# Performance work log

Measured on AMD Instinct MI355X. Metric: run time of the kernel, lower is better.

## Reference

```python
import jax, jax.numpy as jnp
import numpy as np

B, SQ, SK, H, A = 4, 512, 512, 256, 128

def setup_inputs() -> dict:
    key = jax.random.key(0)
    ks = jax.random.split(key, 8)
    s = 1.0 / np.sqrt(H)
    sa = 1.0 / np.sqrt(A)
    return {
        "Q": jax.random.normal(ks[0], (B, SQ, H), dtype=jnp.float32),
        "K": jax.random.normal(ks[1], (B, SK, H), dtype=jnp.float32),
        "V": jax.random.normal(ks[2], (B, SK, H), dtype=jnp.float32),
        "W_q": jax.random.uniform(ks[3], (H, A), jnp.float32, -s, s),
        "W_k": jax.random.uniform(ks[4], (H, A), jnp.float32, -s, s),
        "v": jax.random.uniform(ks[5], (A,), jnp.float32, -sa, sa),
        "W_o": jax.random.uniform(ks[6], (H, H), jnp.float32, -s, s),
        "b_o": jax.random.uniform(ks[7], (H,), jnp.float32, -s, s),
    }

def reference(Q, K, V, W_q, W_k, v, W_o, b_o):
    # Q: (B, Sq, H), K/V: (B, Sk, H)
    Qt = Q @ W_q                      # (B, Sq, A)
    Kt = K @ W_k                      # (B, Sk, A)
    additive = jnp.tanh(Qt[:, :, None, :] + Kt[:, None, :, :])  # (B, Sq, Sk, A)
    scores = jnp.einsum('bqka,a->bqk', additive, v)             # (B, Sq, Sk)
    weights = jax.nn.softmax(scores, axis=-1)                   # (B, Sq, Sk)
    out = jnp.einsum('bqk,bkh->bqh', weights, V)                 # (B, Sq, H)
    out = out @ W_o + b_o
    return (out, weights)
```

## Files before the change

kernel.cpp:

```cpp
#include <hip/hip_runtime.h>
#include <math.h>

#define BB 4
#define SQL 512
#define SKL 512
#define HH 256
#define AA 128

#define PRESCALE 2.8853900817779268f
#define LOG2E    1.4426950408889634f

__device__ inline void fma4(float4& a, float s, const float4& b) {
    a.x = fmaf(s, b.x, a.x); a.y = fmaf(s, b.y, a.y);
    a.z = fmaf(s, b.z, a.z); a.w = fmaf(s, b.w, a.w);
}

template <int CTRL>
__device__ __forceinline__ float dpp_add(float x) {
    int m = __builtin_amdgcn_update_dpp(__float_as_int(x), __float_as_int(x),
                                        CTRL, 0xF, 0xF, false);
    return x + __int_as_float(m);
}
__device__ __forceinline__ float red8(float x) {
    x = dpp_add<0xB1>(x);
    x = dpp_add<0x4E>(x);
    x = dpp_add<0x141>(x);
    return x;
}

__global__ __launch_bounds__(256) void prep_kernel(
    const float* __restrict__ Q, const float* __restrict__ K,
    const float* __restrict__ V,
    const float* __restrict__ Wq, const float* __restrict__ Wk,
    const float* __restrict__ Wo,
    float* __restrict__ Qt, float* __restrict__ Kt, float* __restrict__ VW)
{
    __shared__ float rows[16 * HH];
    __shared__ float wl[64 * 128];
    int tid = threadIdx.x;
    int bid = blockIdx.x;

    const float* X; const float* W; float* Y;
    int ldW, ldY, col0, r0; float scale;
    if (bid < 128)      { X=Q; W=Wq; Y=Qt; ldW=AA; ldY=AA; col0=0; r0=bid*16;       scale=PRESCALE; }
    else if (bid < 256) { X=K; W=Wk; Y=Kt; ldW=AA; ldY=AA; col0=0; r0=(bid-128)*16; scale=PRESCALE; }
    else { int b2=bid-256; X=V; W=Wo; Y=VW; ldW=HH; ldY=HH; col0=(b2&1)*128; r0=(b2>>1)*16; scale=1.0f; }

    {
        const float4* Xv = (const float4*)(X + (size_t)r0 * HH);
        float4* rv = (float4*)rows;
        rv[tid]       = Xv[tid];
        rv[tid + 256] = Xv[tid + 256];
        rv[tid + 512] = Xv[tid + 512];
        rv[tid + 768] = Xv[tid + 768];
    }

    int r  = tid >> 5;
    int c4 = tid & 31;
    float4 accA = {0.f,0.f,0.f,0.f}, accB = {0.f,0.f,0.f,0.f};

    for (int ch = 0; ch < 4; ++ch) {
        __syncthreads();
        {
            const float* Wbase = W + (size_t)(ch * 64) * ldW + col0;
            float4* wv = (float4*)wl;
            #pragma unroll
            for (int it = 0; it < 8; ++it) {
                int l = tid + it * 256;
                wv[l] = *(const float4*)(Wbase + (size_t)(l >> 5) * ldW + ((l & 31) << 2));
            }
        }
        __syncthreads();
        const float* rrowA = rows + r * HH + ch * 64;
        const float* rrowB = rows + (r + 8) * HH + ch * 64;
        #pragma unroll 4
        for (int h4 = 0; h4 < 16; ++h4) {
            float4 ra = *(const float4*)(rrowA + h4 * 4);
            float4 rb = *(const float4*)(rrowB + h4 * 4);
            const float* wbase = wl + (h4 * 4) * 128 + (c4 << 2);
            float4 w0 = *(const float4*)(wbase);
            float4 w1 = *(const float4*)(wbase + 128);
            float4 w2 = *(const float4*)(wbase + 256);
            float4 w3 = *(const float4*)(wbase + 384);
            fma4(accA, ra.x, w0); fma4(accA, ra.y, w1);
            fma4(accA, ra.z, w2); fma4(accA, ra.w, w3);
            fma4(accB, rb.x, w0); fma4(accB, rb.y, w1);
            fma4(accB, rb.z, w2); fma4(accB, rb.w, w3);
        }
    }
    accA.x *= scale; accA.y *= scale; accA.z *= scale; accA.w *= scale;
    accB.x *= scale; accB.y *= scale; accB.z *= scale; accB.w *= scale;
    *(float4*)(Y + (size_t)(r0 + r)     * ldY + col0 + (c4 << 2)) = accA;
    *(float4*)(Y + (size_t)(r0 + r + 8) * ldY + col0 + (c4 << 2)) = accB;
}

__global__ __launch_bounds__(256, 3) void score_kernel(
    const float* __restrict__ Qt, const float* __restrict__ Kt,
    const float* __restrict__ v,  const float* __restrict__ VW,
    const float* __restrict__ bo,
    float* __restrict__ weights,  float* __restrict__ out)
{
    __shared__ float score[4][SKL];
    __shared__ float pout[4][4][HH];

    int tid = threadIdx.x;
    int b  = blockIdx.x >> 7;
    int q0 = (blockIdx.x & 127) << 2;
    int ag = tid & 7;
    int kl = tid >> 3;

    float Eq0[16], Eq1[16], Eq2[16], Eq3[16], v2[16];
    {
        const float4* vp  = (const float4*)(v + ag * 16);
        const float4* qp0 = (const float4*)(Qt + (size_t)(b * SQL + q0)     * AA + ag * 16);
        const float4* qp1 = (const float4*)(Qt + (size_t)(b * SQL + q0 + 1) * AA + ag * 16);
        const float4* qp2 = (const float4*)(Qt + (size_t)(b * SQL + q0 + 2) * AA + ag * 16);
        const float4* qp3 = (const float4*)(Qt + (size_t)(b * SQL + q0 + 3) * AA + ag * 16);
        #pragma unroll
        for (int j4 = 0; j4 < 4; ++j4) {
            float4 vv = vp[j4];
            v2[j4*4+0] = 2.0f*vv.x; v2[j4*4+1] = 2.0f*vv.y;
            v2[j4*4+2] = 2.0f*vv.z; v2[j4*4+3] = 2.0f*vv.w;
            float4 a0 = qp0[j4], a1 = qp1[j4], a2 = qp2[j4], a3 = qp3[j4];
            Eq0[j4*4+0] = __builtin_amdgcn_exp2f(a0.x); Eq0[j4*4+1] = __builtin_amdgcn_exp2f(a0.y);
            Eq0[j4*4+2] = __builtin_amdgcn_exp2f(a0.z); Eq0[j4*4+3] = __builtin_amdgcn_exp2f(a0.w);
            Eq1[j4*4+0] = __builtin_amdgcn_exp2f(a1.x); Eq1[j4*4+1] = __builtin_amdgcn_exp2f(a1.y);
            Eq1[j4*4+2] = __builtin_amdgcn_exp2f(a1.z); Eq1[j4*4+3] = __builtin_amdgcn_exp2f(a1.w);
            Eq2[j4*4+0] = __builtin_amdgcn_exp2f(a2.x); Eq2[j4*4+1] = __builtin_amdgcn_exp2f(a2.y);
            Eq2[j4*4+2] = __builtin_amdgcn_exp2f(a2.z); Eq2[j4*4+3] = __builtin_amdgcn_exp2f(a2.w);
            Eq3[j4*4+0] = __builtin_amdgcn_exp2f(a3.x); Eq3[j4*4+1] = __builtin_amdgcn_exp2f(a3.y);
            Eq3[j4*4+2] = __builtin_amdgcn_exp2f(a3.z); Eq3[j4*4+3] = __builtin_amdgcn_exp2f(a3.w);
        }
    }

    float S_all;
    {
        float ls = 0.f;
        #pragma unroll
        for (int j = 0; j < 16; ++j) ls += v2[j];
        S_all = 0.5f * red8(ls);
    }

    const float* KtB = Kt + (size_t)b * SKL * AA;

    auto loadk = [&](float* kt, int c) {
        const float4* kt4 = (const float4*)(KtB + (size_t)(c * 32 + kl) * AA + ag * 16);
        *(float4*)&kt[0]  = kt4[0];
        *(float4*)&kt[4]  = kt4[1];
        *(float4*)&kt[8]  = kt4[2];
        *(float4*)&kt[12] = kt4[3];
    };

    auto compute = [&](const float* kt, int c) {
        float p0 = 0.f, p1 = 0.f, p2 = 0.f, p3 = 0.f;
        #pragma unroll
        for (int j = 0; j < 16; ++j) {
            float Ek = __builtin_amdgcn_exp2f(kt[j]);
            float r0 = __builtin_amdgcn_rcpf(fmaf(Ek, Eq0[j], 1.0f));
            float r1 = __builtin_amdgcn_rcpf(fmaf(Ek, Eq1[j], 1.0f));
            float r2 = __builtin_amdgcn_rcpf(fmaf(Ek, Eq2[j], 1.0f));
            float r3 = __builtin_amdgcn_rcpf(fmaf(Ek, Eq3[j], 1.0f));
            p0 = fmaf(v2[j], r0, p0);
            p1 = fmaf(v2[j], r1, p1);
            p2 = fmaf(v2[j], r2, p2);
            p3 = fmaf(v2[j], r3, p3);
        }
        p0 = red8(p0); p1 = red8(p1); p2 = red8(p2); p3 = red8(p3);
        if (ag == 0) {
            int k = c * 32 + kl;
            score[0][k] = (S_all - p0) * LOG2E;
            score[1][k] = (S_all - p1) * LOG2E;
            score[2][k] = (S_all - p2) * LOG2E;
            score[3][k] = (S_all - p3) * LOG2E;
        }
    };

    {
        float ktA[16], ktB_[16];
        loadk(ktA, 0);
        #pragma unroll 1
        for (int cc = 0; cc < 8; ++cc) {
            int c0 = cc * 2;
            loadk(ktB_, c0 + 1);
            compute(ktA, c0);
            if (cc != 7) loadk(ktA, c0 + 2);
            compute(ktB_, c0 + 1);
        }
    }
    __syncthreads();

    int wave = tid >> 6, lane = tid & 63;
    {
        int qi = wave;
        float ssum = 0.f;
        #pragma unroll
        for (int it = 0; it < 2; ++it) {
            int k0 = it * 256 + (lane << 2);
            float4 sv = *(float4*)&score[qi][k0];
            sv.x = __builtin_amdgcn_exp2f(sv.x);
            sv.y = __builtin_amdgcn_exp2f(sv.y);
            sv.z = __builtin_amdgcn_exp2f(sv.z);
            sv.w = __builtin_amdgcn_exp2f(sv.w);
            *(float4*)&score[qi][k0] = sv;
            ssum += (sv.x + sv.y) + (sv.z + sv.w);
        }
        #pragma unroll
        for (int off = 32; off; off >>= 1) ssum += __shfl_xor(ssum, off);
        float rinv = 1.0f / ssum;
        size_t rowoff = (size_t)(b * SQL + q0 + qi) * SKL;
        #pragma unroll
        for (int it = 0; it < 2; ++it) {
            int k0 = it * 256 + (lane << 2);
            float4 sv = *(float4*)&score[qi][k0];
            sv.x *= rinv; sv.y *= rinv; sv.z *= rinv; sv.w *= rinv;
            *(float4*)&score[qi][k0] = sv;
            *(float4*)(weights + rowoff + k0) = sv;
        }
    }
    __syncthreads();

    {
        const float4* VWb = (const float4*)(VW + (size_t)b * SKL * HH);
        float4 a0 = {0,0,0,0}, a1 = {0,0,0,0}, a2 = {0,0,0,0}, a3 = {0,0,0,0};
        int kbase = wave * 128;
        #pragma unroll 2
        for (int k4 = 0; k4 < 32; ++k4) {
            int kk = kbase + k4 * 4;
            float4 w0 = *(const float4*)&score[0][kk];
            float4 w1 = *(const float4*)&score[1][kk];
            float4 w2 = *(const float4*)&score[2][kk];
            float4 w3 = *(const float4*)&score[3][kk];
            float4 vw;
            vw = VWb[(size_t)(kk + 0) * (HH/4) + lane];
            fma4(a0, w0.x, vw); fma4(a1, w1.x, vw); fma4(a2, w2.x, vw); fma4(a3, w3.x, vw);
            vw = VWb[(size_t)(kk + 1) * (HH/4) + lane];
            fma4(a0, w0.y, vw); fma4(a1, w1.y, vw); fma4(a2, w2.y, vw); fma4(a3, w3.y, vw);
            vw = VWb[(size_t)(kk + 2) * (HH/4) + lane];
            fma4(a0, w0.z, vw); fma4(a1, w1.z, vw); fma4(a2, w2.z, vw); fma4(a3, w3.z, vw);
            vw = VWb[(size_t)(kk + 3) * (HH/4) + lane];
            fma4(a0, w0.w, vw); fma4(a1, w1.w, vw); fma4(a2, w2.w, vw); fma4(a3, w3.w, vw);
        }
        *(float4*)&pout[wave][0][lane << 2] = a0;
        *(float4*)&pout[wave][1][lane << 2] = a1;
        *(float4*)&pout[wave][2][lane << 2] = a2;
        *(float4*)&pout[wave][3][lane << 2] = a3;
    }
    __syncthreads();
    {
        int h = tid;
        float bias = bo[h];
        #pragma unroll
        for (int qi = 0; qi < 4; ++qi) {
            float s = bias + pout[0][qi][h] + pout[1][qi][h]
                           + pout[2][qi][h] + pout[3][qi][h];
            out[(size_t)(b * SQL + q0 + qi) * HH + h] = s;
        }
    }
}

extern "C" void kernel_launch(void* const* d_in, const int* in_sizes, int n_in,
                              void* d_out, int out_size, void* d_ws, size_t ws_size,
                              hipStream_t stream)
{
    const float* Q  = (const float*)d_in[0];
    const float* K  = (const float*)d_in[1];
    const float* V  = (const float*)d_in[2];
    const float* Wq = (const float*)d_in[3];
    const float* Wk = (const float*)d_in[4];
    const float* v  = (const float*)d_in[5];
    const float* Wo = (const float*)d_in[6];
    const float* bo = (const float*)d_in[7];

    float* out     = (float*)d_out;
    float* weights = out + (size_t)BB * SQL * HH;

    float* Qt = (float*)d_ws;
    float* Kt = Qt + (size_t)BB * SQL * AA;
    float* VW = Kt + (size_t)BB * SKL * AA;

    prep_kernel <<<512, 256, 0, stream>>>(Q, K, V, Wq, Wk, Wo, Qt, Kt, VW);
    score_kernel<<<512, 256, 0, stream>>>(Qt, Kt, v, VW, bo, weights, out);
}
```

Baseline: 115.4 us.

## Process eight queries per block to amortize key exponentials and loads

```diff
diff --git a/kernel.cpp b/kernel.cpp
--- a/kernel.cpp
+++ b/kernel.cpp
@@ -94,42 +94,41 @@
     *(float4*)(Y + (size_t)(r0 + r + 8) * ldY + col0 + (c4 << 2)) = accB;
 }
 
-__global__ __launch_bounds__(256, 3) void score_kernel(
+__global__ __launch_bounds__(512, 2) void score_kernel(
     const float* __restrict__ Qt, const float* __restrict__ Kt,
     const float* __restrict__ v,  const float* __restrict__ VW,
     const float* __restrict__ bo,
     float* __restrict__ weights,  float* __restrict__ out)
 {
-    __shared__ float score[4][SKL];
-    __shared__ float pout[4][4][HH];
+    __shared__ float score[8][SKL];
+    __shared__ float pout[8][4][HH];
 
     int tid = threadIdx.x;
-    int b  = blockIdx.x >> 7;
-    int q0 = (blockIdx.x & 127) << 2;
+    int b  = blockIdx.x >> 6;
+    int q0 = (blockIdx.x & 63) << 3;
     int ag = tid & 7;
     int kl = tid >> 3;
 
-    float Eq0[16], Eq1[16], Eq2[16], Eq3[16], v2[16];
-    {
-        const float4* vp  = (const float4*)(v + ag * 16);
-        const float4* qp0 = (const float4*)(Qt + (size_t)(b * SQL + q0)     * AA + ag * 16);
-        const float4* qp1 = (const float4*)(Qt + (size_t)(b * SQL + q0 + 1) * AA + ag * 16);
-        const float4* qp2 = (const float4*)(Qt + (size_t)(b * SQL + q0 + 2) * AA + ag * 16);
-        const float4* qp3 = (const float4*)(Qt + (size_t)(b * SQL + q0 + 3) * AA + ag * 16);
+    float Eq[8][16], v2[16];
+    {
+        const float4* vp = (const float4*)(v + ag * 16);
         #pragma unroll
         for (int j4 = 0; j4 < 4; ++j4) {
             float4 vv = vp[j4];
             v2[j4*4+0] = 2.0f*vv.x; v2[j4*4+1] = 2.0f*vv.y;
             v2[j4*4+2] = 2.0f*vv.z; v2[j4*4+3] = 2.0f*vv.w;
-            float4 a0 = qp0[j4], a1 = qp1[j4], a2 = qp2[j4], a3 = qp3[j4];
-            Eq0[j4*4+0] = __builtin_amdgcn_exp2f(a0.x); Eq0[j4*4+1] = __builtin_amdgcn_exp2f(a0.y);
-            Eq0[j4*4+2] = __builtin_amdgcn_exp2f(a0.z); Eq0[j4*4+3] = __builtin_amdgcn_exp2f(a0.w);
-            Eq1[j4*4+0] = __builtin_amdgcn_exp2f(a1.x); Eq1[j4*4+1] = __builtin_amdgcn_exp2f(a1.y);
-            Eq1[j4*4+2] = __builtin_amdgcn_exp2f(a1.z); Eq1[j4*4+3] = __builtin_amdgcn_exp2f(a1.w);
-            Eq2[j4*4+0] = __builtin_amdgcn_exp2f(a2.x); Eq2[j4*4+1] = __builtin_amdgcn_exp2f(a2.y);
-            Eq2[j4*4+2] = __builtin_amdgcn_exp2f(a2.z); Eq2[j4*4+3] = __builtin_amdgcn_exp2f(a2.w);
-            Eq3[j4*4+0] = __builtin_amdgcn_exp2f(a3.x); Eq3[j4*4+1] = __builtin_amdgcn_exp2f(a3.y);
-            Eq3[j4*4+2] = __builtin_amdgcn_exp2f(a3.z); Eq3[j4*4+3] = __builtin_amdgcn_exp2f(a3.w);
+        }
+        #pragma unroll
+        for (int q = 0; q < 8; ++q) {
+            const float4* qp = (const float4*)(Qt + (size_t)(b * SQL + q0 + q) * AA + ag * 16);
+            #pragma unroll
+            for (int j4 = 0; j4 < 4; ++j4) {
+                float4 a = qp[j4];
+                Eq[q][j4*4+0] = __builtin_amdgcn_exp2f(a.x);
+                Eq[q][j4*4+1] = __builtin_amdgcn_exp2f(a.y);
+                Eq[q][j4*4+2] = __builtin_amdgcn_exp2f(a.z);
+                Eq[q][j4*4+3] = __builtin_amdgcn_exp2f(a.w);
+            }
         }
     }
 
@@ -144,7 +143,7 @@
     const float* KtB = Kt + (size_t)b * SKL * AA;
 
     auto loadk = [&](float* kt, int c) {
-        const float4* kt4 = (const float4*)(KtB + (size_t)(c * 32 + kl) * AA + ag * 16);
+        const float4* kt4 = (const float4*)(KtB + (size_t)(c * 64 + kl) * AA + ag * 16);
         *(float4*)&kt[0]  = kt4[0];
         *(float4*)&kt[4]  = kt4[1];
         *(float4*)&kt[8]  = kt4[2];
@@ -152,26 +151,26 @@
     };
 
     auto compute = [&](const float* kt, int c) {
-        float p0 = 0.f, p1 = 0.f, p2 = 0.f, p3 = 0.f;
+        float p[8];
+        #pragma unroll
+        for (int q = 0; q < 8; ++q) p[q] = 0.f;
         #pragma unroll
         for (int j = 0; j < 16; ++j) {
             float Ek = __builtin_amdgcn_exp2f(kt[j]);
-            float r0 = __builtin_amdgcn_rcpf(fmaf(Ek, Eq0[j], 1.0f));
-            float r1 = __builtin_amdgcn_rcpf(fmaf(Ek, Eq1[j], 1.0f));
-            float r2 = __builtin_amdgcn_rcpf(fmaf(Ek, Eq2[j], 1.0f));
-            float r3 = __builtin_amdgcn_rcpf(fmaf(Ek, Eq3[j], 1.0f));
-            p0 = fmaf(v2[j], r0, p0);
-            p1 = fmaf(v2[j], r1, p1);
-            p2 = fmaf(v2[j], r2, p2);
-            p3 = fmaf(v2[j], r3, p3);
-        }
-        p0 = red8(p0); p1 = red8(p1); p2 = red8(p2); p3 = red8(p3);
+            float vj = v2[j];
+            #pragma unroll
+            for (int q = 0; q < 8; ++q) {
+                float r = __builtin_amdgcn_rcpf(fmaf(Ek, Eq[q][j], 1.0f));
+                p[q] = fmaf(vj, r, p[q]);
+            }
+        }
+        #pragma unroll
+        for (int q = 0; q < 8; ++q) p[q] = red8(p[q]);
         if (ag == 0) {
-            int k = c * 32 + kl;
-            score[0][k] = (S_all - p0) * LOG2E;
-            score[1][k] = (S_all - p1) * LOG2E;
-            score[2][k] = (S_all - p2) * LOG2E;
-            score[3][k] = (S_all - p3) * LOG2E;
+            int k = c * 64 + kl;
+            #pragma unroll
+            for (int q = 0; q < 8; ++q)
+                score[q][k] = (S_all - p[q]) * LOG2E;
         }
     };
 
@@ -179,11 +178,11 @@
         float ktA[16], ktB_[16];
         loadk(ktA, 0);
         #pragma unroll 1
-        for (int cc = 0; cc < 8; ++cc) {
+        for (int cc = 0; cc < 4; ++cc) {
             int c0 = cc * 2;
             loadk(ktB_, c0 + 1);
             compute(ktA, c0);
-            if (cc != 7) loadk(ktA, c0 + 2);
+            if (cc != 3) loadk(ktA, c0 + 2);
             compute(ktB_, c0 + 1);
         }
     }
@@ -219,42 +218,52 @@
     }
     __syncthreads();
 
-    {
+    float4 acc[8];
+    {
+        #pragma unroll
+        for (int q = 0; q < 8; ++q) acc[q] = make_float4(0.f, 0.f, 0.f, 0.f);
         const float4* VWb = (const float4*)(VW + (size_t)b * SKL * HH);
-        float4 a0 = {0,0,0,0}, a1 = {0,0,0,0}, a2 = {0,0,0,0}, a3 = {0,0,0,0};
-        int kbase = wave * 128;
+        int kbase = wave * 64;
         #pragma unroll 2
-        for (int k4 = 0; k4 < 32; ++k4) {
+        for (int k4 = 0; k4 < 16; ++k4) {
             int kk = kbase + k4 * 4;
-            float4 w0 = *(const float4*)&score[0][kk];
-            float4 w1 = *(const float4*)&score[1][kk];
-            float4 w2 = *(const float4*)&score[2][kk];
-            float4 w3 = *(const float4*)&score[3][kk];
+            float4 w[8];
+            #pragma unroll
+            for (int q = 0; q < 8; ++q) w[q] = *(const float4*)&score[q][kk];
             float4 vw;
             vw = VWb[(size_t)(kk + 0) * (HH/4) + lane];
-            fma4(a0, w0.x, vw); fma4(a1, w1.x, vw); fma4(a2, w2.x, vw); fma4(a3, w3.x, vw);
+            #pragma unroll
+            for (int q = 0; q < 8; ++q) fma4(acc[q], w[q].x, vw);
             vw = VWb[(size_t)(kk + 1) * (HH/4) + lane];
-            fma4(a0, w0.y, vw); fma4(a1, w1.y, vw); fma4(a2, w2.y, vw); fma4(a3, w3.y, vw);
+            #pragma unroll
+            for (int q = 0; q < 8; ++q) fma4(acc[q], w[q].y, vw);
             vw = VWb[(size_t)(kk + 2) * (HH/4) + lane];
-            fma4(a0, w0.z, vw); fma4(a1, w1.z, vw); fma4(a2, w2.z, vw); fma4(a3, w3.z, vw);
+            #pragma unroll
+            for (int q = 0; q < 8; ++q) fma4(acc[q], w[q].z, vw);
             vw = VWb[(size_t)(kk + 3) * (HH/4) + lane];
-            fma4(a0, w0.w, vw); fma4(a1, w1.w, vw); fma4(a2, w2.w, vw); fma4(a3, w3.w, vw);
-        }
-        *(float4*)&pout[wave][0][lane << 2] = a0;
-        *(float4*)&pout[wave][1][lane << 2] = a1;
-        *(float4*)&pout[wave][2][lane << 2] = a2;
-        *(float4*)&pout[wave][3][lane << 2] = a3;
-    }
-    __syncthreads();
-    {
-        int h = tid;
-        float bias = bo[h];
-        #pragma unroll
-        for (int qi = 0; qi < 4; ++qi) {
-            float s = bias + pout[0][qi][h] + pout[1][qi][h]
-                           + pout[2][qi][h] + pout[3][qi][h];
-            out[(size_t)(b * SQL + q0 + qi) * HH + h] = s;
-        }
+            #pragma unroll
+            for (int q = 0; q < 8; ++q) fma4(acc[q], w[q].w, vw);
+        }
+    }
+
+    int h  = tid & 255;
+    int qh = tid >> 8;
+    float bias = bo[h];
+    #pragma unroll
+    for (int rnd = 0; rnd < 2; ++rnd) {
+        #pragma unroll
+        for (int q = 0; q < 4; ++q)
+            *(float4*)&pout[wave][q][lane << 2] = acc[rnd * 4 + q];
+        __syncthreads();
+        #pragma unroll
+        for (int qq = 0; qq < 2; ++qq) {
+            int qi = qh * 2 + qq;
+            float s = bias;
+            #pragma unroll
+            for (int w2 = 0; w2 < 8; ++w2) s += pout[w2][qi][h];
+            out[(size_t)(b * SQL + q0 + rnd * 4 + qi) * HH + h] = s;
+        }
+        __syncthreads();
     }
 }
 
@@ -279,5 +288,5 @@
     float* VW = Kt + (size_t)BB * SKL * AA;
 
     prep_kernel <<<512, 256, 0, stream>>>(Q, K, V, Wq, Wk, Wo, Qt, Kt, VW);
-    score_kernel<<<512, 256, 0, stream>>>(Qt, Kt, v, VW, bo, weights, out);
-}
+    score_kernel<<<256, 512, 0, stream>>>(Qt, Kt, v, VW, bo, weights, out);
+}
```

Result: no change. 114.3 us (-1.0%).
